# Kernel optimization log

Measured on AMD Instinct MI355X. Metric: run time of the kernel, lower is better.

The kernel has to match this reference:

```python
import jax, jax.numpy as jnp
import numpy as np

N_ATOMS = 16384
N_EDGES = 524288
N_MOL = 256
A = 4            # num_pseudo_species
S = 4            # len(unique_numbers)
NMAX = 10        # radial basis size
NSPH = 9         # (l_max+1)^2 with l_max=2
Q = A * NMAX
NL = 3           # l_max+1
F = Q * Q * NL   # 4800 power-spectrum features
CUTOFF = 5.0
AVG_ATOMS = 64.0
SCALE = 1.0
H1, H2 = 512, 512


def _sph_l012(u):
    # real spherical harmonics l=0,1,2 on unit vectors u [E,3] -> [E,9]
    x, y, z = u[:, 0], u[:, 1], u[:, 2]
    c1 = 0.4886025119029199
    c2 = 1.0925484305920792
    return jnp.stack([
        jnp.full_like(x, 0.28209479177387814),
        c1 * y, c1 * z, c1 * x,
        c2 * x * y, c2 * y * z,
        0.31539156525252005 * (3.0 * z * z - 1.0),
        c2 * x * z,
        0.5462742152960396 * (x * x - y * y),
    ], axis=-1)


def _forward(positions, cells, edge_offsets, U, gamma, beta, W1, W2, W3, Wc,
             numbers, edge_indices, batch):
    send, recv = edge_indices[0], edge_indices[1]
    cell_e = cells[batch[send]]                                  # [E,3,3]
    rvec = positions[recv] - positions[send] + jnp.einsum('ek,ekl->el', edge_offsets, cell_e)
    r = jnp.sqrt(jnp.sum(rvec * rvec, axis=-1) + 1e-12)          # [E]
    rhat = rvec / r[:, None]
    fc = 0.5 * (jnp.cos(jnp.pi * r / CUTOFF) + 1.0) * (r < CUTOFF)
    mu = jnp.linspace(0.0, CUTOFF, NMAX)
    sig = CUTOFF / NMAX
    R = jnp.exp(-((r[:, None] - mu) ** 2) / (2.0 * sig * sig)) * fc[:, None]  # [E,NMAX]
    Y = _sph_l012(rhat)                                          # [E,9]
    RY = jnp.einsum('en,ek->enk', R, Y)                          # [E,NMAX,9]
    w = U[:, numbers[send]]                                      # [A,E] pseudo-species mix of neighbor species
    # spherical expansion per atom: c[i,a,n,lm]
    c = jnp.stack([jax.ops.segment_sum(w[a][:, None, None] * RY, recv, num_segments=N_ATOMS)
                   for a in range(A)], axis=1)                   # [N,A,NMAX,9]
    c = c.reshape(N_ATOMS, Q, NSPH)
    # power spectrum: contract over m within each l block, normalize by sqrt(2l+1)
    lblocks = [(0, 1, 1.0), (1, 4, 3.0), (4, 9, 5.0)]
    ps = jnp.stack([jnp.einsum('iqm,ipm->iqp', c[:, :, a:b], c[:, :, a:b]) / jnp.sqrt(nl)
                    for a, b, nl in lblocks], axis=-1).reshape(N_ATOMS, F)
    # layer norm
    mean = ps.mean(axis=-1, keepdims=True)
    var = ps.var(axis=-1, keepdims=True)
    x = (ps - mean) / jnp.sqrt(var + 1e-5) * gamma + beta

    def contract(x, W):
        # species-indexed contraction: per-species weight via combination matrix U
        Wsp = jnp.einsum('as,aio->sio', U, W)                    # [S,in,out]
        out = jnp.zeros((x.shape[0], W.shape[-1]), x.dtype)
        for s in range(S):                                       # small fixed species set
            out = out + jnp.where((numbers == s)[:, None], x @ Wsp[s], 0.0)
        return out

    x = jax.nn.silu(contract(x, W1))
    x = jax.nn.silu(contract(x, W2))
    x = contract(x, W3)                                          # [N,1]
    e = jax.ops.segment_sum(x, batch, num_segments=N_MOL)        # [M,1]
    e = e / jnp.sqrt(float(A)) / AVG_ATOMS
    comp = jax.ops.segment_sum(jax.nn.one_hot(numbers, S, dtype=x.dtype), batch, num_segments=N_MOL)
    return e * SCALE + comp @ Wc.T


def setup_inputs() -> dict:
    key = jax.random.key(0)
    ks = jax.random.split(key, 10)
    positions = jax.random.normal(ks[0], (N_ATOMS, 3), dtype=jnp.float32)
    cells = jnp.zeros((N_MOL, 3, 3), dtype=jnp.float32)
    numbers = jax.random.randint(ks[1], (N_ATOMS,), 0, S)
    edge_indices = jax.random.randint(ks[2], (2, N_EDGES), 0, N_ATOMS)
    edge_offsets = jnp.zeros((N_EDGES, 3), dtype=jnp.float32)
    batch = jnp.sort(jax.random.randint(ks[3], (N_ATOMS,), 0, N_MOL))
    U = jax.random.normal(ks[4], (A, S), dtype=jnp.float32) * 0.5
    gamma = jnp.ones((F,), dtype=jnp.float32)
    beta = jnp.zeros((F,), dtype=jnp.float32)
    W1 = jax.random.normal(ks[5], (A, F, H1), dtype=jnp.float32) / np.sqrt(F)
    W2 = jax.random.normal(ks[6], (A, H1, H2), dtype=jnp.float32) / np.sqrt(H1)
    W3 = jax.random.normal(ks[7], (A, H2, 1), dtype=jnp.float32) / np.sqrt(H2)
    Wc = jax.random.normal(ks[8], (1, S), dtype=jnp.float32) * 0.1
    return {"positions": positions, "cells": cells, "numbers": numbers,
            "edge_indices": edge_indices, "edge_offsets": edge_offsets, "batch": batch,
            "U": U, "gamma": gamma, "beta": beta, "W1": W1, "W2": W2, "W3": W3, "Wc": Wc}


def reference(positions, cells, numbers, edge_indices, edge_offsets, batch,
              U, gamma, beta, W1, W2, W3, Wc):
    return _forward(positions, cells, edge_offsets, U, gamma, beta, W1, W2, W3, Wc,
                    numbers, edge_indices, batch)
```

## Files before the change

### kernel.cpp

```cpp
#include <hip/hip_runtime.h>

#define NA   16384
#define NE   524288
#define NM   256
#define FF   4800
#define FR   2688
#define HH   512
#define NMX  10
#define NSPH 9

typedef __bf16 bf16x8 __attribute__((ext_vector_type(8)));
typedef float  f32x4  __attribute__((ext_vector_type(4)));
typedef unsigned short u16x8 __attribute__((ext_vector_type(8)));

__constant__ int g_ka[22] = {0, 1,1,1,2,2,3, 4,4,4,4,4, 5,5,5,5, 6,6,6, 7,7, 8};
__constant__ int g_kb[22] = {0, 1,2,3,2,3,3, 4,5,6,7,8, 5,6,7,8, 6,7,8, 7,8, 8};

__device__ inline unsigned short f2bf(float x){
  return __builtin_bit_cast(unsigned short, (__bf16)x);
}
__device__ inline float bf2f(unsigned short h){
  unsigned int u = ((unsigned int)h) << 16;
  return __builtin_bit_cast(float, u);
}
__device__ inline void atomic_add_f(float* p, float v){
  __hip_atomic_fetch_add(p, v, __ATOMIC_RELAXED, __HIP_MEMORY_SCOPE_AGENT);
}
__device__ inline void gload16(const void* g, void* l){
  __builtin_amdgcn_global_load_lds(
      (const __attribute__((address_space(1))) unsigned int*)g,
      (__attribute__((address_space(3))) unsigned int*)l, 16, 0, 0);
}
__device__ inline float silu(float x){ return x / (1.f + __expf(-x)); }

__device__ inline void decode_blk(int b, int& qb, int& pb){
  int q = 0, rem = b;
  while (rem >= 10 - q){ rem -= 10 - q; q++; }
  qb = q; pb = q + rem;
}

template<int CNT>
__device__ inline void ps_block(const float* __restrict__ cl, int qb, int pb, int off,
                                float nrm, bool diag, unsigned short* ob){
  float cq[4][CNT], cp[4][CNT];
  #pragma unroll
  for (int i = 0; i < 4; i++)
    #pragma unroll
    for (int k = 0; k < CNT; k++){
      cq[i][k] = cl[(qb*4 + i)*9 + off + k];
      cp[i][k] = cl[(pb*4 + i)*9 + off + k];
    }
  #pragma unroll
  for (int qi = 0; qi < 4; qi++)
    #pragma unroll
    for (int pi = 0; pi < 4; pi++){
      float v = 0.f;
      #pragma unroll
      for (int k = 0; k < CNT; k++) v += cq[qi][k] * cp[pi][k];
      v *= nrm;
      if (diag && qi > pi) v = 0.f;
      ob[qi*4 + pi] = f2bf(v);
    }
}

template<int CNT>
__device__ inline void ps_block_half(const float* __restrict__ cl, int qb, int pb, int off,
                                     float nrm, bool diag, int qh, unsigned short* ob){
  float cq[2][CNT], cp[4][CNT];
  #pragma unroll
  for (int i = 0; i < 2; i++)
    #pragma unroll
    for (int k = 0; k < CNT; k++)
      cq[i][k] = cl[(qb*4 + qh*2 + i)*9 + off + k];
  #pragma unroll
  for (int i = 0; i < 4; i++)
    #pragma unroll
    for (int k = 0; k < CNT; k++)
      cp[i][k] = cl[(pb*4 + i)*9 + off + k];
  #pragma unroll
  for (int qi = 0; qi < 2; qi++)
    #pragma unroll
    for (int pi = 0; pi < 4; pi++){
      int qg = qh*2 + qi;
      float v = 0.f;
      #pragma unroll
      for (int k = 0; k < CNT; k++) v += cq[qi][k] * cp[pi][k];
      v *= nrm;
      if (diag && qg > pi) v = 0.f;
      ob[qi*4 + pi] = f2bf(v);
    }
}

__device__ inline int block_scan_excl(int v, int tid, int* lds){
  int lane = tid & 63, w = tid >> 6;
  int x = v;
  #pragma unroll
  for (int d = 1; d < 64; d <<= 1){
    int y = __shfl_up(x, d, 64);
    if (lane >= d) x += y;
  }
  if (lane == 63) lds[w] = x;
  __syncthreads();
  int wsum = 0;
  for (int i = 0; i < w; i++) wsum += lds[i];
  return wsum + x - v;
}

__global__ __launch_bounds__(256) void k_hist(const int* __restrict__ ei,
                                              const int* __restrict__ numbers,
                                              int* __restrict__ cnt64k,
                                              int* __restrict__ bhist){
  __shared__ int h[4];
  int blk = blockIdx.x, tid = threadIdx.x;
  if (blk < 2048){
    int e = blk * 256 + tid;
    int key = ei[NE + e] * 4 + numbers[ei[e]];
    atomicAdd(&cnt64k[key], 1);
  } else {
    if (tid < 4) h[tid] = 0;
    __syncthreads();
    atomicAdd(&h[numbers[(blk - 2048) * 256 + tid]], 1);
    __syncthreads();
    if (tid < 4) bhist[(blk - 2048) * 4 + tid] = h[tid];
  }
}

__global__ __launch_bounds__(256) void k_scanA(const int* __restrict__ cnt64k,
                                               int* __restrict__ bsum){
  __shared__ int lds[4];
  int tid = threadIdx.x;
  int v = cnt64k[blockIdx.x * 256 + tid];
  int lane = tid & 63;
  #pragma unroll
  for (int m = 32; m; m >>= 1) v += __shfl_xor(v, m, 64);
  if (lane == 0) lds[tid >> 6] = v;
  __syncthreads();
  if (tid == 0) bsum[blockIdx.x] = lds[0] + lds[1] + lds[2] + lds[3];
}

__global__ __launch_bounds__(256) void k_scanB(const int* __restrict__ bsum,
                                               int* __restrict__ boff, int* __restrict__ starts,
                                               const int* __restrict__ bhist,
                                               int* __restrict__ boffs, int* __restrict__ ints){
  __shared__ int lds[4];
  int tid = threadIdx.x;
  int v = bsum[tid];
  int e = block_scan_excl(v, tid, lds);
  boff[tid] = e;
  if (tid == 0){
    starts[65536] = NE;
    int* cnt = ints; int* offs = ints + 8;
    int tot[4] = {0,0,0,0};
    for (int b = 0; b < 64; b++)
      for (int s = 0; s < 4; s++) tot[s] += bhist[b*4 + s];
    int o = 0;
    for (int s = 0; s < 4; s++){ cnt[s] = tot[s]; offs[s] = o; o += tot[s]; }
    offs[4] = o;
    int run[4];
    for (int s = 0; s < 4; s++) run[s] = offs[s];
    for (int b = 0; b < 64; b++)
      for (int s = 0; s < 4; s++){ boffs[b*4 + s] = run[s]; run[s] += bhist[b*4 + s]; }
  }
}

__global__ __launch_bounds__(256) void k_scanC(const int* __restrict__ cnt64k,
                                               const int* __restrict__ boff,
                                               int* __restrict__ starts, int* __restrict__ cursor){
  __shared__ int lds[4];
  int tid = threadIdx.x;
  int bin = blockIdx.x * 256 + tid;
  int v = cnt64k[bin];
  int e = block_scan_excl(v, tid, lds) + boff[blockIdx.x];
  starts[bin] = e;
  cursor[bin] = e;
}

__global__ __launch_bounds__(256) void k_sortperm(const int* __restrict__ ei,
                                                  const int* __restrict__ numbers,
                                                  int* __restrict__ cursor, int* __restrict__ perm){
  int e = blockIdx.x * 256 + threadIdx.x;
  if (e < NE){
    int key = ei[NE + e] * 4 + numbers[ei[e]];
    int p = atomicAdd(&cursor[key], 1);
    perm[p] = e;
  }
}

__global__ __launch_bounds__(256) void k_aplace(const int* __restrict__ numbers,
                                                const int* __restrict__ boffs,
                                                int* __restrict__ list){
  __shared__ int ws[4][4];
  int tid = threadIdx.x, w = tid >> 6, lane = tid & 63;
  int i = blockIdx.x * 256 + tid;
  int sp = numbers[i];
  int rank = 0;
  #pragma unroll
  for (int s = 0; s < 4; s++){
    unsigned long long m = __ballot(sp == s);
    if (s == sp) rank = __popcll(m & (((unsigned long long)1 << lane) - 1));
    if (lane == 0) ws[w][s] = __popcll(m);
  }
  __syncthreads();
  int pre = 0;
  for (int w2 = 0; w2 < w; w2++) pre += ws[w2][sp];
  list[boffs[blockIdx.x * 4 + sp] + pre + rank] = i;
}

__global__ __launch_bounds__(384) void k_atom(
    const float* __restrict__ pos, const float* __restrict__ cells,
    const int* __restrict__ ei, const float* __restrict__ eoff,
    const int* __restrict__ batch, const int* __restrict__ startsK,
    const int* __restrict__ perm, const float* __restrict__ U,
    unsigned short* __restrict__ ps, float* __restrict__ stats)
{
  __shared__ float Rl[64][NMX];
  __shared__ float Yl[64][NSPH];
  __shared__ float csr[360];
  __shared__ float cl[360];
  __shared__ float ul[16];
  int atom = blockIdx.x;
  int tid = threadIdx.x;
  if (tid < 16) ul[tid] = U[tid];
  int e0 = startsK[atom * 4], e1 = startsK[atom * 4 + 4];
  float px = pos[atom*3+0], py = pos[atom*3+1], pz = pos[atom*3+2];
  int sp = tid / 90, n = (tid % 90) / 9, k = tid % 9;
  int aS = 0, aE = 0;
  if (tid < 360){ aS = startsK[atom * 4 + sp]; aE = startsK[atom * 4 + sp + 1]; }
  float acc = 0.f;
  for (int base = e0; base < e1; base += 64){
    int nch = min(64, e1 - base);
    if (tid < nch){
      int e = perm[base + tid];
      int snd = ei[e];
      const float* C = cells + (size_t)batch[snd] * 9;
      float o0 = eoff[e*3+0], o1 = eoff[e*3+1], o2 = eoff[e*3+2];
      float rx = px - pos[snd*3+0] + o0*C[0] + o1*C[3] + o2*C[6];
      float ry = py - pos[snd*3+1] + o0*C[1] + o1*C[4] + o2*C[7];
      float rz = pz - pos[snd*3+2] + o0*C[2] + o1*C[5] + o2*C[8];
      float r = sqrtf(rx*rx + ry*ry + rz*rz + 1e-12f);
      float inv = 1.f / r;
      float hx = rx*inv, hy = ry*inv, hz = rz*inv;
      float fc = (r < 5.f) ? (0.5f * (__cosf(r * 0.6283185307179586f) + 1.f)) : 0.f;
      #pragma unroll
      for (int nn = 0; nn < NMX; nn++){
        float d = r - (5.f/9.f) * (float)nn;
        Rl[tid][nn] = __expf(-2.f * d * d) * fc;
      }
      Yl[tid][0] = 0.28209479177387814f;
      Yl[tid][1] = 0.4886025119029199f * hy;
      Yl[tid][2] = 0.4886025119029199f * hz;
      Yl[tid][3] = 0.4886025119029199f * hx;
      Yl[tid][4] = 1.0925484305920792f * hx * hy;
      Yl[tid][5] = 1.0925484305920792f * hy * hz;
      Yl[tid][6] = 0.31539156525252005f * (3.f * hz * hz - 1.f);
      Yl[tid][7] = 1.0925484305920792f * hx * hz;
      Yl[tid][8] = 0.5462742152960396f * (hx * hx - hy * hy);
    }
    __syncthreads();
    if (tid < 360){
      int lo2 = max(aS, base), hi2 = min(aE, base + nch);
      for (int e = lo2; e < hi2; e++){
        int j = e - base;
        acc += Rl[j][n] * Yl[j][k];
      }
    }
    __syncthreads();
  }
  if (tid < 360) csr[tid] = acc;
  __syncthreads();
  if (tid < 360){
    int a = tid / 90, nk = tid % 90;
    cl[tid] = ul[a*4+0]*csr[nk] + ul[a*4+1]*csr[90+nk]
            + ul[a*4+2]*csr[180+nk] + ul[a*4+3]*csr[270+nk];
  }
  __syncthreads();
  int w6 = tid >> 6, b = tid & 63;
  if (w6 <= 3 && b < 55){
    int l = (w6 < 2) ? 2 : 1;
    int qh = w6 & 1;
    int qb, pb;
    decode_blk(b, qb, pb);
    bool diag = (qb == pb);
    unsigned short ob[8];
    if (l == 2) ps_block_half<5>(cl, qb, pb, 4, 0.4472135954999579f, diag, qh, ob);
    else        ps_block_half<3>(cl, qb, pb, 1, 0.5773502691896258f, diag, qh, ob);
    unsigned short* dst = ps + (size_t)atom * FR + b * 48 + l * 16 + qh * 8;
    *reinterpret_cast<u16x8*>(dst) = *(const u16x8*)ob;
  } else if (w6 == 4 && b < 55){
    int qb, pb;
    decode_blk(b, qb, pb);
    bool diag = (qb == pb);
    unsigned short ob[16];
    ps_block<1>(cl, qb, pb, 0, 1.f, diag, ob);
    unsigned short* dst = ps + (size_t)atom * FR + b * 48;
    *reinterpret_cast<u16x8*>(dst)     = *(const u16x8*)&ob[0];
    *reinterpret_cast<u16x8*>(dst + 8) = *(const u16x8*)&ob[8];
  } else if (w6 == 5){
    if (b < 6){
      unsigned short zb[8] = {0,0,0,0,0,0,0,0};
      *reinterpret_cast<u16x8*>(ps + (size_t)atom * FR + 2640 + b * 8) = *(const u16x8*)zb;
    }
    float c1 = 0.f, c2 = 0.f;
    if (b >= 8 && b < 17){
      int kk = b - 8;
      float S = 0.f;
      for (int q = 0; q < 40; q++) S += cl[q*9 + kk];
      float nrm = (kk == 0) ? 1.f : ((kk < 4) ? 0.5773502691896258f : 0.4472135954999579f);
      c1 = nrm * S * S;
    } else if (b >= 24 && b < 46){
      int j = b - 24;
      int ka = g_ka[j], kb = g_kb[j];
      float G = 0.f;
      for (int q = 0; q < 40; q++) G += cl[q*9 + ka] * cl[q*9 + kb];
      float n2 = (ka == 0) ? 1.f : ((ka < 4) ? (1.f/3.f) : 0.2f);
      float mul = (ka == kb) ? 1.f : 2.f;
      c2 = n2 * mul * G * G;
    }
    #pragma unroll
    for (int m = 32; m; m >>= 1){ c1 += __shfl_xor(c1, m, 64); c2 += __shfl_xor(c2, m, 64); }
    if (b == 0){
      float mean = c1 * (1.f / FF);
      float var = c2 * (1.f / FF) - mean * mean;
      var = fmaxf(var, 0.f);
      stats[2*atom]   = mean;
      stats[2*atom+1] = rsqrtf(var + 1e-5f);
    }
  }
}

__global__ __launch_bounds__(256) void k_wg3(
    const float* __restrict__ W1, const float* __restrict__ U,
    const float* __restrict__ gamma, const float* __restrict__ beta,
    unsigned short* __restrict__ Wg, float* __restrict__ gW, float* __restrict__ bW)
{
  __shared__ unsigned short og[4][64][64];
  int n0 = blockIdx.x * 64, f0 = blockIdx.y * 64;
  int tid = threadIdx.x, ni = tid & 63;
  float u[4][4];
  #pragma unroll
  for (int a = 0; a < 4; a++)
    #pragma unroll
    for (int s = 0; s < 4; s++) u[a][s] = U[a*4 + s];
  float gs[4] = {0,0,0,0}, bs[4] = {0,0,0,0};
  for (int rep = 0; rep < 16; rep++){
    int fi = rep * 4 + (tid >> 6);
    int fp = f0 + fi;
    int b = fp / 48, r = fp % 48;
    int l = r >> 4, qi = (r >> 2) & 3, pi = r & 3;
    float tg[4] = {0,0,0,0}, tb[4] = {0,0,0,0};
    if (b < 55){
      int qb, pb;
      decode_blk(b, qb, pb);
      bool zero = (qb == pb) && (qi > pi);
      if (!zero){
        int q = qb*4 + qi, p = pb*4 + pi;
        int fa = (q * 40 + p) * 3 + l;
        float ga = gamma[fa], ba = beta[fa];
        float wm[4] = {0,0,0,0};
        #pragma unroll
        for (int a = 0; a < 4; a++){
          float wa = W1[(size_t)a * FF * 512 + (size_t)fa * 512 + n0 + ni];
          #pragma unroll
          for (int s = 0; s < 4; s++) wm[s] += u[a][s] * wa;
        }
        #pragma unroll
        for (int s = 0; s < 4; s++){ tg[s] = ga * wm[s]; tb[s] = ba * wm[s]; }
        if (p != q){
          int fb = (p * 40 + q) * 3 + l;
          float gb = gamma[fb], bb = beta[fb];
          float wn[4] = {0,0,0,0};
          #pragma unroll
          for (int a = 0; a < 4; a++){
            float wb = W1[(size_t)a * FF * 512 + (size_t)fb * 512 + n0 + ni];
            #pragma unroll
            for (int s = 0; s < 4; s++) wn[s] += u[a][s] * wb;
          }
          #pragma unroll
          for (int s = 0; s < 4; s++){ tg[s] += gb * wn[s]; tb[s] += bb * wn[s]; }
        }
      }
    }
    #pragma unroll
    for (int s = 0; s < 4; s++){
      og[s][fi][ni] = f2bf(tg[s]);
      gs[s] += tg[s];
      bs[s] += tb[s];
    }
  }
  #pragma unroll
  for (int s = 0; s < 4; s++){
    atomic_add_f(&gW[s * 512 + n0 + ni], gs[s]);
    atomic_add_f(&bW[s * 512 + n0 + ni], bs[s]);
  }
  __syncthreads();
  for (int it = 0; it < 8; it++){
    int idx = it * 256 + tid;
    int c = idx & 7;
    int rrow = idx >> 3;
    int s = rrow >> 6, nn = rrow & 63;
    unsigned short o[8];
    #pragma unroll
    for (int j = 0; j < 8; j++) o[j] = og[s][c*8 + j][nn];
    *reinterpret_cast<u16x8*>(&Wg[((size_t)s * 512 + n0 + nn) * FR + f0 + c * 8]) = *(const u16x8*)o;
  }
}

__global__ __launch_bounds__(256) void k_w2t(
    const float* __restrict__ W2, const float* __restrict__ U,
    unsigned short* __restrict__ W2t)
{
  __shared__ float t[64][65];
  int n0 = blockIdx.x * 64, k0 = blockIdx.y * 64, s = blockIdx.z;
  float u0 = U[s], u1 = U[4+s], u2 = U[8+s], u3 = U[12+s];
  int tid = threadIdx.x;
  #pragma unroll 4
  for (int rep = 0; rep < 16; rep++){
    int idx = rep * 256 + tid;
    int ki = idx >> 6, ni = idx & 63;
    size_t base = (size_t)(k0 + ki) * 512 + (n0 + ni);
    t[ki][ni] = u0*W2[base] + u1*W2[base + 512*512]
              + u2*W2[base + 2*512*512] + u3*W2[base + 3*512*512];
  }
  __syncthreads();
  #pragma unroll 4
  for (int rep = 0; rep < 16; rep++){
    int idx = rep * 256 + tid;
    int ni = idx >> 6, ki = idx & 63;
    W2t[((size_t)s * 512 + n0 + ni) * 512 + k0 + ki] = f2bf(t[ki][ni]);
  }
}

__global__ void k_w3(const float* __restrict__ W3, const float* __restrict__ U,
                     float* __restrict__ W3s)
{
  int idx = blockIdx.x * 256 + threadIdx.x;
  if (idx < 4 * 512){
    int s = idx >> 9, k = idx & 511;
    W3s[idx] = U[s]*W3[k] + U[4+s]*W3[512+k] + U[8+s]*W3[2*512+k] + U[12+s]*W3[3*512+k];
  }
}

template<int EPI, int NSPLIT>
__global__ __launch_bounds__(256) void k_gemm(
    const unsigned short* __restrict__ Ag, int lda, int K,
    const unsigned short* __restrict__ Btg,
    const int* __restrict__ list, const int* __restrict__ offs, const int* __restrict__ cnt,
    unsigned short* __restrict__ pout,
    const float* __restrict__ W3s, float* __restrict__ pacc)
{
  __shared__ alignas(16) char smem[32768];
  const int NV = 4 * NSPLIT;
  int b = blockIdx.x;
  int y = (b & 7) + 8 * (b / (8 * NV));
  int v = (b >> 3) % NV;
  int x = v & 3, kh = v >> 2;

  int s = 0, t = y;
  for (; s < 4; s++){
    int nts = (cnt[s] + 127) >> 7;
    if (t < nts) break;
    t -= nts;
  }
  if (s >= 4) return;
  int cntS = cnt[s], offS = offs[s];
  int rt = t, n0 = x * 128;
  int tid = threadIdx.x, w = tid >> 6, lane = tid & 63;
  int wr = w >> 1, wc = w & 1;

  const unsigned short* Bts = Btg + (size_t)s * 512 * K;
  const unsigned short* gA[4];
  const unsigned short* gB[4];
  char* lA[4];
  char* lB[4];
  #pragma unroll
  for (int it = 0; it < 4; it++){
    int g = it * 4 + w;
    int idx = g * 64 + lane;
    int row = idx >> 3, ch = idx & 7;
    int cg = ch ^ (row & 7);
    int gr = rt * 128 + row; gr = gr < cntS ? gr : cntS - 1;
    int atom = list[offS + gr];
    gA[it] = Ag + (size_t)atom * lda + cg * 8;
    lA[it] = smem + g * 1024;
    gB[it] = Bts + (size_t)(n0 + row) * K + cg * 8;
    lB[it] = smem + 16384 + g * 1024;
  }

  int hi = lane >> 4, lo = lane & 15;
  f32x4 acc[4][4];
  #pragma unroll
  for (int mi = 0; mi < 4; mi++)
    #pragma unroll
    for (int ni = 0; ni < 4; ni++)
      #pragma unroll
      for (int r = 0; r < 4; r++) acc[mi][ni][r] = 0.f;

  int abase[4], a7[4], bbase[4], b7[4];
  #pragma unroll
  for (int mi = 0; mi < 4; mi++){ int row = wr*64 + mi*16 + lo; abase[mi] = row*128; a7[mi] = row & 7; }
  #pragma unroll
  for (int ni = 0; ni < 4; ni++){ int row = wc*64 + ni*16 + lo; bbase[ni] = 16384 + row*128; b7[ni] = row & 7; }

  int nk = K / 64;
  int k0 = ((nk * kh) / NSPLIT) * 64;
  int k1 = ((nk * (kh + 1)) / NSPLIT) * 64;

  for (int kt = k0; kt < k1; kt += 64){
    #pragma unroll
    for (int it = 0; it < 4; it++) gload16(gA[it] + kt, lA[it]);
    #pragma unroll
    for (int it = 0; it < 4; it++) gload16(gB[it] + kt, lB[it]);
    __syncthreads();
    #pragma unroll
    for (int kk = 0; kk < 2; kk++){
      bf16x8 af[4], bfr[4];
      #pragma unroll
      for (int mi = 0; mi < 4; mi++)
        af[mi] = *(const bf16x8*)(smem + abase[mi] + (((kk*4 + hi) ^ a7[mi]) << 4));
      #pragma unroll
      for (int ni = 0; ni < 4; ni++)
        bfr[ni] = *(const bf16x8*)(smem + bbase[ni] + (((kk*4 + hi) ^ b7[ni]) << 4));
      #pragma unroll
      for (int mi = 0; mi < 4; mi++)
        #pragma unroll
        for (int ni = 0; ni < 4; ni++)
          acc[mi][ni] = __builtin_amdgcn_mfma_f32_16x16x32_bf16(af[mi], bfr[ni], acc[mi][ni], 0, 0, 0);
    }
    __syncthreads();
  }

  int gn[4];
  #pragma unroll
  for (int ni = 0; ni < 4; ni++) gn[ni] = n0 + wc*64 + ni*16 + lo;

  if (EPI == 0){
    #pragma unroll
    for (int mi = 0; mi < 4; mi++){
      #pragma unroll
      for (int j = 0; j < 4; j++){
        int gr = rt*128 + wr*64 + mi*16 + hi*4 + j;
        if (gr < cntS){
          int atom = list[offS + gr];
          #pragma unroll
          for (int ni = 0; ni < 4; ni++)
            pout[((size_t)kh * NA + atom) * 512 + gn[ni]] = f2bf(acc[mi][ni][j]);
        }
      }
    }
  } else {
    float w3v[4];
    #pragma unroll
    for (int ni = 0; ni < 4; ni++) w3v[ni] = W3s[s * 512 + gn[ni]];
    float* pslot = pacc + (size_t)(x * 2 + wc) * NA;
    #pragma unroll
    for (int mi = 0; mi < 4; mi++){
      #pragma unroll
      for (int j = 0; j < 4; j++){
        int gr = rt*128 + wr*64 + mi*16 + hi*4 + j;
        if (gr < cntS){
          int atom = list[offS + gr];
          float pdot = 0.f;
          #pragma unroll
          for (int ni = 0; ni < 4; ni++)
            pdot += silu(acc[mi][ni][j]) * w3v[ni];
          pdot += __shfl_xor(pdot, 1, 16);
          pdot += __shfl_xor(pdot, 2, 16);
          pdot += __shfl_xor(pdot, 4, 16);
          pdot += __shfl_xor(pdot, 8, 16);
          if (lo == 0) pslot[atom] = pdot;
        }
      }
    }
  }
}

__global__ __launch_bounds__(256) void k_epi(
    const unsigned short* __restrict__ pbuf, const float* __restrict__ stats,
    const float* __restrict__ gW, const float* __restrict__ bW,
    const int* __restrict__ numbers, unsigned short* __restrict__ h1)
{
  int w = threadIdx.x >> 6, lane = threadIdx.x & 63;
  int atom = blockIdx.x * 4 + w;
  int s = numbers[atom];
  float mean = stats[2*atom], rstd = stats[2*atom+1];
  int c0 = lane * 8;
  u16x8 a0 = *reinterpret_cast<const u16x8*>(pbuf + (size_t)atom * 512 + c0);
  u16x8 a1 = *reinterpret_cast<const u16x8*>(pbuf + (size_t)(NA + atom) * 512 + c0);
  u16x8 a2 = *reinterpret_cast<const u16x8*>(pbuf + (size_t)(2*NA + atom) * 512 + c0);
  u16x8 a3 = *reinterpret_cast<const u16x8*>(pbuf + (size_t)(3*NA + atom) * 512 + c0);
  unsigned short o[8];
  #pragma unroll
  for (int j = 0; j < 8; j++){
    int c = c0 + j;
    float acc = (bf2f(a0[j]) + bf2f(a1[j])) + (bf2f(a2[j]) + bf2f(a3[j]));
    float vv = rstd * acc + bW[s*512 + c] - mean * rstd * gW[s*512 + c];
    o[j] = f2bf(silu(vv));
  }
  *reinterpret_cast<u16x8*>(h1 + (size_t)atom * 512 + c0) = *(const u16x8*)o;
}

__global__ __launch_bounds__(256) void k_final2(
    const float* __restrict__ pacc, const int* __restrict__ numbers,
    const int* __restrict__ batch, const float* __restrict__ Wc,
    float* __restrict__ molOut)
{
  int atom = blockIdx.x * 256 + threadIdx.x;
  int lane = threadIdx.x & 63;
  float sum = 0.f;
  #pragma unroll
  for (int p = 0; p < 8; p++) sum += pacc[(size_t)p * NA + atom];
  float val = sum * (1.f / 128.f) + Wc[numbers[atom]];
  int mol = batch[atom];
  int m0 = __shfl(mol, 0, 64);
  int m63 = __shfl(mol, 63, 64);
  if (m0 == m63){
    #pragma unroll
    for (int m = 32; m; m >>= 1) val += __shfl_xor(val, m, 64);
    if (lane == 0) atomic_add_f(&molOut[mol], val);
  } else {
    atomic_add_f(&molOut[mol], val);
  }
}

extern "C" void kernel_launch(void* const* d_in, const int* in_sizes, int n_in,
                              void* d_out, int out_size, void* d_ws, size_t ws_size,
                              hipStream_t stream)
{
  const float* pos     = (const float*)d_in[0];
  const float* cells   = (const float*)d_in[1];
  const int*   numbers = (const int*)d_in[2];
  const int*   ei      = (const int*)d_in[3];
  const float* eoff    = (const float*)d_in[4];
  const int*   batch   = (const int*)d_in[5];
  const float* U       = (const float*)d_in[6];
  const float* gamma   = (const float*)d_in[7];
  const float* beta    = (const float*)d_in[8];
  const float* W1      = (const float*)d_in[9];
  const float* W2      = (const float*)d_in[10];
  const float* W3      = (const float*)d_in[11];
  const float* Wc      = (const float*)d_in[12];
  float* out = (float*)d_out;

  char* ws = (char*)d_ws;
  size_t off = 0;
  auto alloc = [&](size_t bytes) -> void* {
    void* p = ws + off;
    off += (bytes + 255) & ~(size_t)255;
    return p;
  };
  unsigned short* ps   = (unsigned short*)alloc((size_t)NA * FR * 2);
  unsigned short* pbuf = (unsigned short*)alloc((size_t)4 * NA * 512 * 2);
  float* stats         = (float*)alloc((size_t)NA * 2 * 4);
  unsigned short* Wg1  = (unsigned short*)alloc((size_t)4 * 512 * FR * 2);
  unsigned short* W2t  = (unsigned short*)alloc((size_t)4 * 512 * 512 * 2);
  float* W3s           = (float*)alloc(4 * 512 * 4);
  unsigned short* h1   = (unsigned short*)alloc((size_t)NA * 512 * 2);
  float* pacc          = (float*)alloc((size_t)8 * NA * 4);
  int* list            = (int*)alloc(NA * 4);
  int* perm            = (int*)alloc((size_t)NE * 4);
  int* startsK         = (int*)alloc((65536 + 1) * 4);
  int* cnt64k          = (int*)alloc(65536 * 4);
  float* gW            = (float*)alloc(4 * 512 * 4);
  float* bW            = (float*)alloc(4 * 512 * 4);
  int* cursor64k       = (int*)alloc(65536 * 4);
  int* bsum            = (int*)alloc(256 * 4);
  int* boff            = (int*)alloc(256 * 4);
  int* bhist           = (int*)alloc(64 * 4 * 4);
  int* boffs           = (int*)alloc(64 * 4 * 4);
  int* ints            = (int*)alloc(64);
  int* cnt = ints; int* offs = ints + 8;

  hipMemsetAsync(cnt64k, 0, 65536 * 4 + 2 * 4 * 512 * 4, stream);
  hipMemsetAsync(out, 0, (size_t)out_size * 4, stream);

  k_hist<<<2048 + 64, 256, 0, stream>>>(ei, numbers, cnt64k, bhist);
  k_scanA<<<256, 256, 0, stream>>>(cnt64k, bsum);
  k_scanB<<<1, 256, 0, stream>>>(bsum, boff, startsK, bhist, boffs, ints);
  k_scanC<<<256, 256, 0, stream>>>(cnt64k, boff, startsK, cursor64k);
  k_sortperm<<<NE / 256, 256, 0, stream>>>(ei, numbers, cursor64k, perm);
  k_aplace<<<NA / 256, 256, 0, stream>>>(numbers, boffs, list);

  k_atom<<<NA, 384, 0, stream>>>(pos, cells, ei, eoff, batch, startsK, perm, U, ps, stats);

  k_wg3<<<dim3(8, 42), 256, 0, stream>>>(W1, U, gamma, beta, Wg1, gW, bW);
  k_w2t<<<dim3(8, 8, 4), 256, 0, stream>>>(W2, U, W2t);
  k_w3<<<8, 256, 0, stream>>>(W3, U, W3s);

  k_gemm<0, 4><<<2176, 256, 0, stream>>>(ps, FR, FR, Wg1, list, offs, cnt,
                                         pbuf, nullptr, nullptr);
  k_epi<<<NA / 4, 256, 0, stream>>>(pbuf, stats, gW, bW, numbers, h1);

  k_gemm<2, 1><<<544, 256, 0, stream>>>(h1, 512, 512, W2t, list, offs, cnt,
                                        nullptr, W3s, pacc);
  k_final2<<<NA / 256, 256, 0, stream>>>(pacc, numbers, batch, Wc, out);
}
```

Baseline: 314.6 us.

## Widen per-atom kernel to 512 threads with 128-edge chunks

Raises the per-atom block from 384 to 512 threads so each species gets its own 128-lane group, and loads edges in chunks of 128 instead of 64. This halves the number of chunk iterations and barriers for atoms with many neighbours. The power-spectrum stage is redistributed so the l=2 blocks are split four ways across four waves rather than two, which shortens the longest wave. In exchange, 38 lanes per species group sit idle during accumulation and LDS use per block grows, which may reduce the number of blocks resident per CU.

```diff
diff --git a/kernel.cpp b/kernel.cpp
--- a/kernel.cpp
+++ b/kernel.cpp
@@ -12,6 +12,7 @@
 typedef __bf16 bf16x8 __attribute__((ext_vector_type(8)));
 typedef float  f32x4  __attribute__((ext_vector_type(4)));
 typedef unsigned short u16x8 __attribute__((ext_vector_type(8)));
+typedef unsigned short u16x4 __attribute__((ext_vector_type(4)));
 
 __constant__ int g_ka[22] = {0, 1,1,1,2,2,3, 4,4,4,4,4, 5,5,5,5, 6,6,6, 7,7, 8};
 __constant__ int g_kb[22] = {0, 1,2,3,2,3,3, 4,5,6,7,8, 5,6,7,8, 6,7,8, 7,8, 8};
@@ -89,6 +90,28 @@
       if (diag && qg > pi) v = 0.f;
       ob[qi*4 + pi] = f2bf(v);
     }
+}
+
+template<int CNT>
+__device__ inline void ps_block_quarter(const float* __restrict__ cl, int qb, int pb, int off,
+                                        float nrm, bool diag, int qi, unsigned short* ob){
+  float cq[CNT], cp[4][CNT];
+  #pragma unroll
+  for (int k = 0; k < CNT; k++) cq[k] = cl[(qb*4 + qi)*9 + off + k];
+  #pragma unroll
+  for (int i = 0; i < 4; i++)
+    #pragma unroll
+    for (int k = 0; k < CNT; k++)
+      cp[i][k] = cl[(pb*4 + i)*9 + off + k];
+  #pragma unroll
+  for (int pi = 0; pi < 4; pi++){
+    float v = 0.f;
+    #pragma unroll
+    for (int k = 0; k < CNT; k++) v += cq[k] * cp[pi][k];
+    v *= nrm;
+    if (diag && qi > pi) v = 0.f;
+    ob[pi] = f2bf(v);
+  }
 }
 
 __device__ inline int block_scan_excl(int v, int tid, int* lds){
@@ -206,15 +229,15 @@
   list[boffs[blockIdx.x * 4 + sp] + pre + rank] = i;
 }
 
-__global__ __launch_bounds__(384) void k_atom(
+__global__ __launch_bounds__(512) void k_atom(
     const float* __restrict__ pos, const float* __restrict__ cells,
     const int* __restrict__ ei, const float* __restrict__ eoff,
     const int* __restrict__ batch, const int* __restrict__ startsK,
     const int* __restrict__ perm, const float* __restrict__ U,
     unsigned short* __restrict__ ps, float* __restrict__ stats)
 {
-  __shared__ float Rl[64][NMX];
-  __shared__ float Yl[64][NSPH];
+  __shared__ float Rl[128][NMX];
+  __shared__ float Yl[128][NSPH];
   __shared__ float csr[360];
   __shared__ float cl[360];
   __shared__ float ul[16];
@@ -223,12 +246,12 @@
   if (tid < 16) ul[tid] = U[tid];
   int e0 = startsK[atom * 4], e1 = startsK[atom * 4 + 4];
   float px = pos[atom*3+0], py = pos[atom*3+1], pz = pos[atom*3+2];
-  int sp = tid / 90, n = (tid % 90) / 9, k = tid % 9;
-  int aS = 0, aE = 0;
-  if (tid < 360){ aS = startsK[atom * 4 + sp]; aE = startsK[atom * 4 + sp + 1]; }
+  int sp = tid >> 7, nk = tid & 127;
+  int n = nk / 9, k = nk - n * 9;
+  int aS = startsK[atom * 4 + sp], aE = startsK[atom * 4 + sp + 1];
   float acc = 0.f;
-  for (int base = e0; base < e1; base += 64){
-    int nch = min(64, e1 - base);
+  for (int base = e0; base < e1; base += 128){
+    int nch = min(128, e1 - base);
     if (tid < nch){
       int e = perm[base + tid];
       int snd = ei[e];
@@ -257,7 +280,7 @@
       Yl[tid][8] = 0.5462742152960396f * (hx * hx - hy * hy);
     }
     __syncthreads();
-    if (tid < 360){
+    if (nk < 90){
       int lo2 = max(aS, base), hi2 = min(aE, base + nch);
       for (int e = lo2; e < hi2; e++){
         int j = e - base;
@@ -266,27 +289,33 @@
     }
     __syncthreads();
   }
-  if (tid < 360) csr[tid] = acc;
+  if (nk < 90) csr[sp * 90 + nk] = acc;
   __syncthreads();
   if (tid < 360){
-    int a = tid / 90, nk = tid % 90;
-    cl[tid] = ul[a*4+0]*csr[nk] + ul[a*4+1]*csr[90+nk]
-            + ul[a*4+2]*csr[180+nk] + ul[a*4+3]*csr[270+nk];
+    int a = tid / 90, nq = tid % 90;
+    cl[tid] = ul[a*4+0]*csr[nq] + ul[a*4+1]*csr[90+nq]
+            + ul[a*4+2]*csr[180+nq] + ul[a*4+3]*csr[270+nq];
   }
   __syncthreads();
-  int w6 = tid >> 6, b = tid & 63;
-  if (w6 <= 3 && b < 55){
-    int l = (w6 < 2) ? 2 : 1;
-    int qh = w6 & 1;
+  int w8 = tid >> 6, b = tid & 63;
+  if (w8 < 4 && b < 55){
+    int qb, pb;
+    decode_blk(b, qb, pb);
+    bool diag = (qb == pb);
+    unsigned short ob[4];
+    ps_block_quarter<5>(cl, qb, pb, 4, 0.4472135954999579f, diag, w8, ob);
+    unsigned short* dst = ps + (size_t)atom * FR + b * 48 + 32 + w8 * 4;
+    *reinterpret_cast<u16x4*>(dst) = *(const u16x4*)ob;
+  } else if ((w8 == 4 || w8 == 5) && b < 55){
+    int qh = w8 - 4;
     int qb, pb;
     decode_blk(b, qb, pb);
     bool diag = (qb == pb);
     unsigned short ob[8];
-    if (l == 2) ps_block_half<5>(cl, qb, pb, 4, 0.4472135954999579f, diag, qh, ob);
-    else        ps_block_half<3>(cl, qb, pb, 1, 0.5773502691896258f, diag, qh, ob);
-    unsigned short* dst = ps + (size_t)atom * FR + b * 48 + l * 16 + qh * 8;
+    ps_block_half<3>(cl, qb, pb, 1, 0.5773502691896258f, diag, qh, ob);
+    unsigned short* dst = ps + (size_t)atom * FR + b * 48 + 16 + qh * 8;
     *reinterpret_cast<u16x8*>(dst) = *(const u16x8*)ob;
-  } else if (w6 == 4 && b < 55){
+  } else if (w8 == 6 && b < 55){
     int qb, pb;
     decode_blk(b, qb, pb);
     bool diag = (qb == pb);
@@ -295,7 +324,7 @@
     unsigned short* dst = ps + (size_t)atom * FR + b * 48;
     *reinterpret_cast<u16x8*>(dst)     = *(const u16x8*)&ob[0];
     *reinterpret_cast<u16x8*>(dst + 8) = *(const u16x8*)&ob[8];
-  } else if (w6 == 5){
+  } else if (w8 == 7){
     if (b < 6){
       unsigned short zb[8] = {0,0,0,0,0,0,0,0};
       *reinterpret_cast<u16x8*>(ps + (size_t)atom * FR + 2640 + b * 8) = *(const u16x8*)zb;
@@ -680,7 +709,7 @@
   k_sortperm<<<NE / 256, 256, 0, stream>>>(ei, numbers, cursor64k, perm);
   k_aplace<<<NA / 256, 256, 0, stream>>>(numbers, boffs, list);
 
-  k_atom<<<NA, 384, 0, stream>>>(pos, cells, ei, eoff, batch, startsK, perm, U, ps, stats);
+  k_atom<<<NA, 512, 0, stream>>>(pos, cells, ei, eoff, batch, startsK, perm, U, ps, stats);
 
   k_wg3<<<dim3(8, 42), 256, 0, stream>>>(W1, U, gamma, beta, Wg1, gW, bW);
   k_w2t<<<dim3(8, 8, 4), 256, 0, stream>>>(W2, U, W2t);
```

Measured after the change: 324.7 us. 3.2% more time.
